# Optimization experiments

Hardware: AMD Instinct MI355X
Metric: run time of the kernel (lower is better)

The kernel has to match this reference:

```python
import jax, jax.numpy as jnp
import numpy as np

B, C, T = 4, 1024, 1024
H = 16
HD = C // H            # head dim = 64
D_ROPE = HD // 2       # rotary dims = 32 (k_channels * 0.5)


def setup_inputs() -> dict:
    key = jax.random.key(0)
    ks = jax.random.split(key, 10)
    s = 1.0 / np.sqrt(C)
    return {
        "x": jax.random.normal(ks[0], (B, C, T), jnp.float32),
        "c": jax.random.normal(ks[1], (B, C, T), jnp.float32),
        "attn_mask": jnp.ones((B, 1, T, T), jnp.int32),
        "Wq": jax.random.normal(ks[2], (C, C), jnp.float32) * s,
        "bq": jax.random.normal(ks[3], (C,), jnp.float32) * 0.01,
        "Wk": jax.random.normal(ks[4], (C, C), jnp.float32) * s,
        "bk": jax.random.normal(ks[5], (C,), jnp.float32) * 0.01,
        "Wv": jax.random.normal(ks[6], (C, C), jnp.float32) * s,
        "bv": jax.random.normal(ks[7], (C,), jnp.float32) * 0.01,
        "Wo": jax.random.normal(ks[8], (C, C), jnp.float32) * s,
        "bo": jax.random.normal(ks[9], (C,), jnp.float32) * 0.01,
    }


def _rope(xh):
    # xh: [b, h, t, hd]; rotate first D_ROPE dims (labml-style), pass the rest
    t = xh.shape[2]
    half = D_ROPE // 2
    theta = 1.0 / (10000.0 ** (jnp.arange(0, half, dtype=jnp.float32) * 2.0 / D_ROPE))
    ang = jnp.arange(t, dtype=jnp.float32)[:, None] * theta[None, :]       # [t, half]
    cos = jnp.concatenate([jnp.cos(ang), jnp.cos(ang)], axis=-1)           # [t, D_ROPE]
    sin = jnp.concatenate([jnp.sin(ang), jnp.sin(ang)], axis=-1)
    x_rope, x_pass = xh[..., :D_ROPE], xh[..., D_ROPE:]
    neg_half = jnp.concatenate([-x_rope[..., half:], x_rope[..., :half]], axis=-1)
    x_rope = x_rope * cos + neg_half * sin
    return jnp.concatenate([x_rope, x_pass], axis=-1)


def _split_heads(z):
    # [b, (h hd), t] -> [b, h, t, hd]
    b, _, t = z.shape
    return z.reshape(b, H, HD, t).transpose(0, 1, 3, 2)


def reference(x, c, attn_mask, Wq, bq, Wk, bk, Wv, bv, Wo, bo):
    # 1x1 conv == pointwise linear over channel dim
    q = jnp.einsum('oc,bct->bot', Wq, x) + bq[None, :, None]
    k = jnp.einsum('oc,bct->bot', Wk, c) + bk[None, :, None]
    v = jnp.einsum('oc,bct->bot', Wv, c) + bv[None, :, None]

    qh = _rope(_split_heads(q))   # [b, h, tq, hd]
    kh = _rope(_split_heads(k))   # [b, h, ts, hd]
    vh = _split_heads(v)          # [b, h, ts, hd]

    scores = jnp.einsum('bhtd,bhsd->bhts', qh, kh) / jnp.sqrt(jnp.float32(HD))
    scores = jnp.where(attn_mask == 0, jnp.float32(-10000.0), scores)
    p = jax.nn.softmax(scores, axis=-1)
    out = jnp.einsum('bhts,bhsd->bhtd', p, vh)          # [b, h, tq, hd]

    # [b,h,t,hd] -> [b,h,hd,t] -> [b, C, t]
    out = out.transpose(0, 1, 3, 2).reshape(out.shape[0], C, out.shape[2])
    return jnp.einsum('oc,bct->bot', Wo, out) + bo[None, :, None]
```

## Files before the change

### kernel.cpp

```cpp
#include <hip/hip_runtime.h>
#include <math.h>

#define BB 4
#define CC 1024
#define TT 1024
#define HH 16
#define HDD 64

typedef float floatx4 __attribute__((ext_vector_type(4)));
typedef __bf16 bf16x8 __attribute__((ext_vector_type(8)));
typedef __bf16 bf16x4 __attribute__((ext_vector_type(4)));

__device__ __forceinline__ void gld_lds16(const __bf16* g, __bf16* l) {
    __builtin_amdgcn_global_load_lds(
        (__attribute__((address_space(1))) void*)(g),
        (__attribute__((address_space(3))) void*)(l), 16, 0, 0);
}

__global__ __launch_bounds__(256) void prep_kernel(
    const float* __restrict__ x, const float* __restrict__ c,
    __bf16* __restrict__ xT, __bf16* __restrict__ cT,
    const float* __restrict__ Wq, const float* __restrict__ Wk,
    const float* __restrict__ Wv, const float* __restrict__ Wo,
    __bf16* __restrict__ Wqb, __bf16* __restrict__ Wkb,
    __bf16* __restrict__ Wvb, __bf16* __restrict__ Wob) {
    __shared__ float tile[64][65];
    int tid = threadIdx.x;
    int z = blockIdx.z;
    if (z == 8) {
        const float* srcs[4] = {Wq, Wk, Wv, Wo};
        __bf16* dsts[4] = {Wqb, Wkb, Wvb, Wob};
        int bid = blockIdx.y * 16 + blockIdx.x;
        int mi = bid >> 6;
        const float* s = srcs[mi];
        __bf16* d = dsts[mi];
        int base = (bid & 63) * 16384;
#pragma unroll
        for (int u = 0; u < 16; ++u) {
            int idx = base + u * 1024 + tid * 4;
            float4 v4 = *(const float4*)(s + idx);
            bf16x4 o;
            o[0] = (__bf16)v4.x; o[1] = (__bf16)v4.y;
            o[2] = (__bf16)v4.z; o[3] = (__bf16)v4.w;
            *(bf16x4*)(d + idx) = o;
        }
        return;
    }
    const float* src = (z < 4) ? x : c;
    __bf16* dst = (z < 4) ? xT : cT;
    int b = z & 3;
    int t0 = blockIdx.x * 64, c0 = blockIdx.y * 64;
    int r = tid >> 2, s16 = (tid & 3) * 16;
    const float* sp = src + (size_t)b * CC * TT + (size_t)(c0 + r) * TT + t0 + s16;
    float4 a0 = *(const float4*)(sp + 0);
    float4 a1 = *(const float4*)(sp + 4);
    float4 a2 = *(const float4*)(sp + 8);
    float4 a3 = *(const float4*)(sp + 12);
    float* tr = &tile[r][s16];
    tr[0] = a0.x; tr[1] = a0.y; tr[2]  = a0.z; tr[3]  = a0.w;
    tr[4] = a1.x; tr[5] = a1.y; tr[6]  = a1.z; tr[7]  = a1.w;
    tr[8] = a2.x; tr[9] = a2.y; tr[10] = a2.z; tr[11] = a2.w;
    tr[12] = a3.x; tr[13] = a3.y; tr[14] = a3.z; tr[15] = a3.w;
    __syncthreads();
    bf16x8 p0, p1;
#pragma unroll
    for (int j = 0; j < 8; ++j) {
        p0[j] = (__bf16)tile[s16 + j][r];
        p1[j] = (__bf16)tile[s16 + 8 + j][r];
    }
    __bf16* dp = dst + (size_t)b * TT * CC + (size_t)(t0 + r) * CC + c0 + s16;
    *(bf16x8*)(dp) = p0;
    *(bf16x8*)(dp + 8) = p1;
}

template <int EPI, typename OutT>
__device__ __forceinline__ void gemm_bt64(
    __bf16* smem, const __bf16* __restrict__ A, const __bf16* __restrict__ Bt,
    const float* __restrict__ bias, OutT* __restrict__ out, float qs) {
    __bf16* Al = smem;
    __bf16* Bl = smem + 8192;
    const int tid = threadIdx.x, l = tid & 63, w = tid >> 6;
    const int m0 = blockIdx.y * 128, n0 = blockIdx.x * 128;
    const int wm = (w >> 1) * 64, wn = (w & 1) * 64;
    const int lm = l & 15, lq = l >> 4;
    const int s7 = lm & 7;
    const int cg0 = (lq ^ s7) * 8, cg1 = ((4 + lq) ^ s7) * 8;
    const int srow = l >> 3, scg = l & 7;
    const int gcg = (scg ^ srow) * 8;

    const __bf16* ga = A + (size_t)(m0 + w * 32 + srow) * 1024 + gcg;
    const __bf16* gb = Bt + (size_t)(n0 + w * 32 + srow) * 1024 + gcg;
    __bf16* adst = Al + w * 32 * 64;
    __bf16* bdst = Bl + w * 32 * 64;

    floatx4 acc[4][4];
#pragma unroll
    for (int i = 0; i < 4; ++i)
#pragma unroll
        for (int j = 0; j < 4; ++j) acc[i][j] = (floatx4){0.f, 0.f, 0.f, 0.f};

#pragma unroll 1
    for (int kt = 0; kt < 16; ++kt) {
        __syncthreads();
#pragma unroll
        for (int c2 = 0; c2 < 4; ++c2) {
            gld_lds16(ga + (size_t)c2 * 8 * 1024, adst + c2 * 512);
            gld_lds16(gb + (size_t)c2 * 8 * 1024, bdst + c2 * 512);
        }
        ga += 64;
        gb += 64;
        __syncthreads();
#pragma unroll
        for (int kk = 0; kk < 2; ++kk) {
            const int cg = kk ? cg1 : cg0;
            bf16x8 af[4], bfr[4];
#pragma unroll
            for (int i = 0; i < 4; ++i) af[i] = *(bf16x8*)&Al[(wm + i * 16 + lm) * 64 + cg];
#pragma unroll
            for (int j = 0; j < 4; ++j) bfr[j] = *(bf16x8*)&Bl[(wn + j * 16 + lm) * 64 + cg];
#pragma unroll
            for (int i = 0; i < 4; ++i)
#pragma unroll
                for (int j = 0; j < 4; ++j)
                    acc[i][j] = __builtin_amdgcn_mfma_f32_16x16x32_bf16(af[i], bfr[j], acc[i][j], 0, 0, 0);
        }
    }

    if (EPI == 1) {
        float b4[4][4];
#pragma unroll
        for (int i = 0; i < 4; ++i)
#pragma unroll
            for (int r = 0; r < 4; ++r) b4[i][r] = bias[m0 + wm + i * 16 + lq * 4 + r];
#pragma unroll
        for (int r = 0; r < 4; ++r) {
            float theta = __expf(-0.57564627f * (float)(lq * 4 + r));
#pragma unroll
            for (int j = 0; j < 4; ++j) {
                float ang = (float)(n0 + wn + j * 16 + lm) * theta;
                float cs = __cosf(ang), sn = __sinf(ang);
                float a0 = acc[0][j][r] + b4[0][r];
                float a1 = acc[1][j][r] + b4[1][r];
                acc[0][j][r] = (a0 * cs - a1 * sn) * qs;
                acc[1][j][r] = (a1 * cs + a0 * sn) * qs;
                acc[2][j][r] = (acc[2][j][r] + b4[2][r]) * qs;
                acc[3][j][r] = (acc[3][j][r] + b4[3][r]) * qs;
            }
        }
        __syncthreads();
        const int hl = wm >> 6;
#pragma unroll
        for (int j = 0; j < 4; ++j) {
            int row = hl * 128 + wn + j * 16 + lm;
#pragma unroll
            for (int i = 0; i < 4; ++i) {
                bf16x4 pk;
#pragma unroll
                for (int r = 0; r < 4; ++r) pk[r] = (__bf16)acc[i][j][r];
                *(bf16x4*)&smem[row * 72 + i * 16 + lq * 4] = pk;
            }
        }
        __syncthreads();
        const size_t hbase = (size_t)(m0 >> 6) * (TT * 64);
#pragma unroll
        for (int it = 0; it < 8; ++it) {
            int chunk = tid + 256 * it;
            int row = chunk >> 3, off = (chunk & 7) * 8;
            int hh = row >> 7, t = n0 + (row & 127);
            *(bf16x8*)&out[hbase + (size_t)hh * (TT * 64) + (size_t)t * 64 + off] =
                *(bf16x8*)&smem[row * 72 + off];
        }
    } else {
#pragma unroll
        for (int i = 0; i < 4; ++i) {
            int mbase = m0 + wm + i * 16 + lq * 4;
#pragma unroll
            for (int r = 0; r < 4; ++r) {
                float bv = bias[mbase + r];
                size_t rowoff = (size_t)(mbase + r) * 1024 + n0 + wn + lm;
#pragma unroll
                for (int j = 0; j < 4; ++j)
                    out[rowoff + j * 16] = (OutT)(acc[i][j][r] + bv);
            }
        }
    }
}

__global__ __launch_bounds__(256) void gemm_qkv_kernel(
    const __bf16* __restrict__ Wqb, const __bf16* __restrict__ Wkb, const __bf16* __restrict__ Wvb,
    const __bf16* __restrict__ xT, const __bf16* __restrict__ cT,
    const float* __restrict__ bq, const float* __restrict__ bk, const float* __restrict__ bv,
    __bf16* __restrict__ qhb, __bf16* __restrict__ khb, __bf16* __restrict__ vb) {
    __shared__ __bf16 smem[18432];
    int z = blockIdx.z, which = z >> 2, b = z & 3;
    if (which == 0) {
        gemm_bt64<1, __bf16>(smem, Wqb, xT + (size_t)b * TT * CC, bq,
                             qhb + (size_t)b * HH * TT * 64, 0.18033688f);
    } else if (which == 1) {
        gemm_bt64<1, __bf16>(smem, Wkb, cT + (size_t)b * TT * CC, bk,
                             khb + (size_t)b * HH * TT * 64, 1.0f);
    } else {
        gemm_bt64<0, __bf16>(smem, Wvb, cT + (size_t)b * TT * CC, bv,
                             vb + (size_t)b * CC * TT, 1.0f);
    }
}

__global__ __launch_bounds__(256) void gemm_out_kernel(
    const __bf16* __restrict__ Wob, const __bf16* __restrict__ attT,
    const float* __restrict__ bo, float* __restrict__ out) {
    __shared__ __bf16 smem[18432];
    int b = blockIdx.z;
    gemm_bt64<2, float>(smem, Wob, attT + (size_t)b * TT * CC, bo,
                        out + (size_t)b * CC * TT, 1.0f);
}

#define ATTN_STAGE(KB, VB)                      \
    do {                                        \
        gld_lds16(kg, &KB[w * 1024]);           \
        gld_lds16(kg + 512, &KB[w * 1024 + 512]); \
        gld_lds16(vg, &VB[w * 1024]);           \
        gld_lds16(vg + 8 * TT, &VB[w * 1024 + 512]); \
        kg += 4096;                             \
        vg += 64;                               \
    } while (0)

#define ATTN_STEP(KB, VB)                                                            \
    do {                                                                             \
        floatx4 sT[2][4];                                                            \
        _Pragma("unroll") for (int i = 0; i < 4; ++i) {                              \
            sT[0][i] = (floatx4){0.f, 0.f, 0.f, 0.f};                                \
            sT[1][i] = (floatx4){0.f, 0.f, 0.f, 0.f};                                \
        }                                                                            \
        _Pragma("unroll") for (int i = 0; i < 4; ++i) {                              \
            bf16x8 kf0 = *(bf16x8*)&KB[koff + i * 1024 + cg0];                       \
            bf16x8 kf1 = *(bf16x8*)&KB[koff + i * 1024 + cg1];                       \
            sT[0][i] = __builtin_amdgcn_mfma_f32_16x16x32_bf16(kf0, qf00, sT[0][i], 0, 0, 0); \
            sT[0][i] = __builtin_amdgcn_mfma_f32_16x16x32_bf16(kf1, qf01, sT[0][i], 0, 0, 0); \
            sT[1][i] = __builtin_amdgcn_mfma_f32_16x16x32_bf16(kf0, qf10, sT[1][i], 0, 0, 0); \
            sT[1][i] = __builtin_amdgcn_mfma_f32_16x16x32_bf16(kf1, qf11, sT[1][i], 0, 0, 0); \
        }                                                                            \
        float rs0 = 0.f, rs1 = 0.f;                                                  \
        _Pragma("unroll") for (int i = 0; i < 4; ++i)                                \
            _Pragma("unroll") for (int r = 0; r < 4; ++r) {                          \
                float e0 = __builtin_amdgcn_exp2f(sT[0][i][r]);                      \
                float e1 = __builtin_amdgcn_exp2f(sT[1][i][r]);                      \
                sT[0][i][r] = e0; rs0 += e0;                                         \
                sT[1][i][r] = e1; rs1 += e1;                                         \
            }                                                                        \
        rs0 += __shfl_xor(rs0, 16, 64); rs0 += __shfl_xor(rs0, 32, 64);              \
        rs1 += __shfl_xor(rs1, 16, 64); rs1 += __shfl_xor(rs1, 32, 64);              \
        l_acc0 += rs0; l_acc1 += rs1;                                                \
        _Pragma("unroll") for (int i = 0; i < 4; ++i) {                              \
            bf16x4 p0, p1;                                                           \
            _Pragma("unroll") for (int r = 0; r < 4; ++r) {                          \
                p0[r] = (__bf16)sT[0][i][r];                                         \
                p1[r] = (__bf16)sT[1][i][r];                                         \
            }                                                                        \
            *(bf16x4*)&pwl[i * 16 + lq * 4] = p0;                                    \
            *(bf16x4*)&pwl[1152 + i * 16 + lq * 4] = p1;                             \
        }                                                                            \
        asm volatile("s_waitcnt lgkmcnt(0)" ::: "memory");                           \
        _Pragma("unroll") for (int ss = 0; ss < 2; ++ss) {                           \
            bf16x8 ap0 = *(bf16x8*)&pwl[ss * 32 + lq * 8];                           \
            bf16x8 ap1 = *(bf16x8*)&pwl[1152 + ss * 32 + lq * 8];                    \
            const int cgv = ss ? cg1 : cg0;                                          \
            _Pragma("unroll") for (int j = 0; j < 4; ++j) {                          \
                bf16x8 vf = *(bf16x8*)&VB[koff + j * 1024 + cgv];                    \
                o_acc[0][j] = __builtin_amdgcn_mfma_f32_16x16x32_bf16(ap0, vf, o_acc[0][j], 0, 0, 0); \
                o_acc[1][j] = __builtin_amdgcn_mfma_f32_16x16x32_bf16(ap1, vf, o_acc[1][j], 0, 0, 0); \
            }                                                                        \
        }                                                                            \
    } while (0)

__global__ __launch_bounds__(256, 4) void attn_kernel(
    const __bf16* __restrict__ qh, const __bf16* __restrict__ kh,
    const __bf16* __restrict__ v, __bf16* __restrict__ attT) {
    const int bh = blockIdx.x, b = bh >> 4, h = bh & 15;
    const int tq0 = blockIdx.y * 128;
    const int tid = threadIdx.x, l = tid & 63, w = tid >> 6;
    const int lm = l & 15, lq = l >> 4;

    __shared__ __bf16 k0[4096], v0[4096], k1[4096], v1[4096];
    __shared__ __bf16 p_lds[9216];

    const int cg0 = (lq ^ (lm & 7)) * 8;
    const int cg1 = ((4 + lq) ^ (lm & 7)) * 8;
    const int koff = lm * 64;
    __bf16* pwl = p_lds + w * 2304 + lm * 72;

    const __bf16* qbase = qh + (size_t)bh * TT * 64 + (size_t)(tq0 + w * 32 + lm) * 64 + lq * 8;
    bf16x8 qf00 = *(const bf16x8*)(qbase);
    bf16x8 qf01 = *(const bf16x8*)(qbase + 32);
    bf16x8 qf10 = *(const bf16x8*)(qbase + 1024);
    bf16x8 qf11 = *(const bf16x8*)(qbase + 1024 + 32);

    const int srow = l >> 3, scg = l & 7;
    const int gcg = (scg ^ srow) * 8;
    const __bf16* kg = kh + (size_t)bh * TT * 64 + (size_t)(w * 16 + srow) * 64 + gcg;
    const __bf16* vg = v + (size_t)b * CC * TT + (size_t)(h * 64 + w * 16 + srow) * TT + gcg;

    floatx4 o_acc[2][4];
#pragma unroll
    for (int j = 0; j < 4; ++j) {
        o_acc[0][j] = (floatx4){0.f, 0.f, 0.f, 0.f};
        o_acc[1][j] = (floatx4){0.f, 0.f, 0.f, 0.f};
    }
    float l_acc0 = 0.f, l_acc1 = 0.f;

    ATTN_STAGE(k0, v0);
#pragma unroll 1
    for (int st = 0; st < 16; st += 2) {
        __syncthreads();
        ATTN_STAGE(k1, v1);
        ATTN_STEP(k0, v0);
        __syncthreads();
        if (st + 2 < 16) ATTN_STAGE(k0, v0);
        ATTN_STEP(k1, v1);
    }

    float inv0[4], inv1[4];
#pragma unroll
    for (int r = 0; r < 4; ++r) {
        inv0[r] = 1.0f / __shfl(l_acc0, lq * 4 + r, 64);
        inv1[r] = 1.0f / __shfl(l_acc1, lq * 4 + r, 64);
    }
#pragma unroll
    for (int j = 0; j < 4; ++j)
#pragma unroll
        for (int r = 0; r < 4; ++r) {
            p_lds[(w * 32 + lq * 4 + r) * 72 + j * 16 + lm] = (__bf16)(o_acc[0][j][r] * inv0[r]);
            p_lds[(w * 32 + 16 + lq * 4 + r) * 72 + j * 16 + lm] = (__bf16)(o_acc[1][j][r] * inv1[r]);
        }
    __syncthreads();
    __bf16* obase = attT + (size_t)b * TT * CC + (size_t)tq0 * CC + h * 64;
#pragma unroll
    for (int it = 0; it < 4; ++it) {
        int chunk = tid + 256 * it;
        int row = chunk >> 3, off = (chunk & 7) * 8;
        *(bf16x8*)&obase[(size_t)row * CC + off] = *(bf16x8*)&p_lds[row * 72 + off];
    }
}

extern "C" void kernel_launch(void* const* d_in, const int* in_sizes, int n_in,
                              void* d_out, int out_size, void* d_ws, size_t ws_size,
                              hipStream_t stream) {
    const float* x = (const float*)d_in[0];
    const float* c = (const float*)d_in[1];
    const float* Wq = (const float*)d_in[3];
    const float* bq = (const float*)d_in[4];
    const float* Wk = (const float*)d_in[5];
    const float* bk = (const float*)d_in[6];
    const float* Wv = (const float*)d_in[7];
    const float* bv = (const float*)d_in[8];
    const float* Wo = (const float*)d_in[9];
    const float* bo = (const float*)d_in[10];

    const size_t MB = 1024ull * 1024ull;
    char* ws = (char*)d_ws;
    __bf16* Wqb  = (__bf16*)(ws + 0 * MB);
    __bf16* Wkb  = (__bf16*)(ws + 2 * MB);
    __bf16* Wvb  = (__bf16*)(ws + 4 * MB);
    __bf16* Wob  = (__bf16*)(ws + 6 * MB);
    __bf16* xT   = (__bf16*)(ws + 8 * MB);
    __bf16* cT   = (__bf16*)(ws + 16 * MB);
    __bf16* qhb  = (__bf16*)(ws + 24 * MB);
    __bf16* khb  = (__bf16*)(ws + 32 * MB);
    __bf16* vbuf = (__bf16*)(ws + 40 * MB);
    __bf16* attT = (__bf16*)(ws + 48 * MB);

    prep_kernel<<<dim3(16, 16, 9), 256, 0, stream>>>(x, c, xT, cT, Wq, Wk, Wv, Wo,
                                                     Wqb, Wkb, Wvb, Wob);
    gemm_qkv_kernel<<<dim3(8, 8, 12), 256, 0, stream>>>(Wqb, Wkb, Wvb, xT, cT, bq, bk, bv,
                                                        qhb, khb, vbuf);
    attn_kernel<<<dim3(64, 8), 256, 0, stream>>>(qhb, khb, vbuf, attT);
    gemm_out_kernel<<<dim3(8, 8, 4), 256, 0, stream>>>(Wob, attT, bo, (float*)d_out);
}
```

Before: 214.7 us.

## Double-buffer GEMM LDS tiles with 32-wide K steps to overlap loads

The shared GEMM routine now uses K tiles of 32 instead of 64 and keeps two LDS buffers. The next tile's global-to-LDS load is issued before the current tile is computed, and the XOR swizzle changes to match the 32-element rows. This aims to hide global load latency behind the MFMA work and to halve the number of barriers per unit of load/compute overlap. In exchange there are twice as many loop iterations, each with less compute per barrier.

```diff
diff --git a/kernel.cpp b/kernel.cpp
--- a/kernel.cpp
+++ b/kernel.cpp
@@ -74,24 +74,43 @@
 }
 
 template <int EPI, typename OutT>
-__device__ __forceinline__ void gemm_bt64(
+__device__ __forceinline__ void gemm_bt32(
     __bf16* smem, const __bf16* __restrict__ A, const __bf16* __restrict__ Bt,
     const float* __restrict__ bias, OutT* __restrict__ out, float qs) {
-    __bf16* Al = smem;
-    __bf16* Bl = smem + 8192;
     const int tid = threadIdx.x, l = tid & 63, w = tid >> 6;
     const int m0 = blockIdx.y * 128, n0 = blockIdx.x * 128;
     const int wm = (w >> 1) * 64, wn = (w & 1) * 64;
     const int lm = l & 15, lq = l >> 4;
-    const int s7 = lm & 7;
-    const int cg0 = (lq ^ s7) * 8, cg1 = ((4 + lq) ^ s7) * 8;
-    const int srow = l >> 3, scg = l & 7;
-    const int gcg = (scg ^ srow) * 8;
+    const int v8 = (lq ^ (lm & 3)) * 8;
+    const int srow = l >> 2;
+    const int gcg = ((l & 3) ^ ((l >> 2) & 3)) * 8;
 
     const __bf16* ga = A + (size_t)(m0 + w * 32 + srow) * 1024 + gcg;
     const __bf16* gb = Bt + (size_t)(n0 + w * 32 + srow) * 1024 + gcg;
-    __bf16* adst = Al + w * 32 * 64;
-    __bf16* bdst = Bl + w * 32 * 64;
+    __bf16* adst = smem + w * 1024;
+    __bf16* bdst = smem + 4096 + w * 1024;
+
+#define GSTAGE(BUFOFF)                                       \
+    do {                                                     \
+        gld_lds16(ga, adst + (BUFOFF));                      \
+        gld_lds16(ga + 16 * 1024, adst + (BUFOFF) + 512);    \
+        gld_lds16(gb, bdst + (BUFOFF));                      \
+        gld_lds16(gb + 16 * 1024, bdst + (BUFOFF) + 512);    \
+        ga += 32;                                            \
+        gb += 32;                                            \
+    } while (0)
+
+#define GCOMP(BUFOFF)                                                          \
+    do {                                                                       \
+        bf16x8 af[4], bfr[4];                                                  \
+        _Pragma("unroll") for (int i = 0; i < 4; ++i)                          \
+            af[i] = *(bf16x8*)&smem[(BUFOFF) + (wm + i * 16 + lm) * 32 + v8];  \
+        _Pragma("unroll") for (int j = 0; j < 4; ++j)                          \
+            bfr[j] = *(bf16x8*)&smem[(BUFOFF) + 4096 + (wn + j * 16 + lm) * 32 + v8]; \
+        _Pragma("unroll") for (int i = 0; i < 4; ++i)                          \
+            _Pragma("unroll") for (int j = 0; j < 4; ++j)                      \
+                acc[i][j] = __builtin_amdgcn_mfma_f32_16x16x32_bf16(af[i], bfr[j], acc[i][j], 0, 0, 0); \
+    } while (0)
 
     floatx4 acc[4][4];
 #pragma unroll
@@ -99,32 +118,18 @@
 #pragma unroll
         for (int j = 0; j < 4; ++j) acc[i][j] = (floatx4){0.f, 0.f, 0.f, 0.f};
 
+    GSTAGE(0);
 #pragma unroll 1
-    for (int kt = 0; kt < 16; ++kt) {
-        __syncthreads();
-#pragma unroll
-        for (int c2 = 0; c2 < 4; ++c2) {
-            gld_lds16(ga + (size_t)c2 * 8 * 1024, adst + c2 * 512);
-            gld_lds16(gb + (size_t)c2 * 8 * 1024, bdst + c2 * 512);
-        }
-        ga += 64;
-        gb += 64;
-        __syncthreads();
-#pragma unroll
-        for (int kk = 0; kk < 2; ++kk) {
-            const int cg = kk ? cg1 : cg0;
-            bf16x8 af[4], bfr[4];
-#pragma unroll
-            for (int i = 0; i < 4; ++i) af[i] = *(bf16x8*)&Al[(wm + i * 16 + lm) * 64 + cg];
-#pragma unroll
-            for (int j = 0; j < 4; ++j) bfr[j] = *(bf16x8*)&Bl[(wn + j * 16 + lm) * 64 + cg];
-#pragma unroll
-            for (int i = 0; i < 4; ++i)
-#pragma unroll
-                for (int j = 0; j < 4; ++j)
-                    acc[i][j] = __builtin_amdgcn_mfma_f32_16x16x32_bf16(af[i], bfr[j], acc[i][j], 0, 0, 0);
-        }
-    }
+    for (int kt = 0; kt < 32; kt += 2) {
+        __syncthreads();
+        GSTAGE(8192);
+        GCOMP(0);
+        __syncthreads();
+        if (kt + 2 < 32) GSTAGE(0);
+        GCOMP(8192);
+    }
+#undef GSTAGE
+#undef GCOMP
 
     if (EPI == 1) {
         float b4[4][4];
@@ -194,13 +199,13 @@
     __shared__ __bf16 smem[18432];
     int z = blockIdx.z, which = z >> 2, b = z & 3;
     if (which == 0) {
-        gemm_bt64<1, __bf16>(smem, Wqb, xT + (size_t)b * TT * CC, bq,
+        gemm_bt32<1, __bf16>(smem, Wqb, xT + (size_t)b * TT * CC, bq,
                              qhb + (size_t)b * HH * TT * 64, 0.18033688f);
     } else if (which == 1) {
-        gemm_bt64<1, __bf16>(smem, Wkb, cT + (size_t)b * TT * CC, bk,
+        gemm_bt32<1, __bf16>(smem, Wkb, cT + (size_t)b * TT * CC, bk,
                              khb + (size_t)b * HH * TT * 64, 1.0f);
     } else {
-        gemm_bt64<0, __bf16>(smem, Wvb, cT + (size_t)b * TT * CC, bv,
+        gemm_bt32<0, __bf16>(smem, Wvb, cT + (size_t)b * TT * CC, bv,
                              vb + (size_t)b * CC * TT, 1.0f);
     }
 }
@@ -210,7 +215,7 @@
     const float* __restrict__ bo, float* __restrict__ out) {
     __shared__ __bf16 smem[18432];
     int b = blockIdx.z;
-    gemm_bt64<2, float>(smem, Wob, attT + (size_t)b * TT * CC, bo,
+    gemm_bt32<2, float>(smem, Wob, attT + (size_t)b * TT * CC, bo,
                         out + (size_t)b * CC * TT, 1.0f);
 }
 
```

Result: faster. 204.6 us (-4.7%).
